# Kernel optimization log

Hardware: AMD Instinct MI355X
Metric: run time of the kernel (lower is better)

Reference implementation:

```python
import jax, jax.numpy as jnp
import numpy as np

MARGIN = 0.3
EPS = 1e-12

def setup_inputs() -> dict:
    key = jax.random.key(0)
    k1, k2 = jax.random.split(key)
    B, D, NUM_IDS = 1024, 2048, 256
    features = jax.random.normal(k1, (B, D), dtype=jnp.float32)
    labels = jax.random.randint(k2, (B,), 0, NUM_IDS, dtype=jnp.int64)
    return {"features": features, "labels": labels}

def _pairwise_euclidean(features):
    # dist^2 = |x_i|^2 + |x_j|^2 - 2 x_i . x_j, clamped then sqrt (as in torch ref)
    sq = jnp.sum(features * features, axis=1)  # [B]
    d2 = sq[:, None] + sq[None, :] - 2.0 * (features @ features.T)
    return jnp.sqrt(jnp.maximum(d2, EPS))

def reference(features, labels):
    B = features.shape[0]
    dist = _pairwise_euclidean(features)  # [B, B]
    eq = labels[None, :] == labels[:, None]  # [B, B]; eq[i] == labels_equal row i
    eye = jnp.eye(B, dtype=bool)
    pos_mask = eq & ~eye
    neg_mask = ~eq
    neg_inf = jnp.float32(-jnp.inf)
    pos_inf = jnp.float32(jnp.inf)
    hardest_pos = jnp.max(jnp.where(pos_mask, dist, neg_inf), axis=1)  # [B]
    hardest_neg = jnp.min(jnp.where(neg_mask, dist, pos_inf), axis=1)  # [B]
    valid = jnp.any(pos_mask, axis=1) & jnp.any(neg_mask, axis=1)  # rows contributing a triplet
    per_row = jax.nn.relu(hardest_pos - hardest_neg + MARGIN)
    per_row = jnp.where(valid, per_row, 0.0)
    n_valid = jnp.sum(valid)
    loss = jnp.sum(per_row) / jnp.maximum(n_valid, 1).astype(per_row.dtype)
    num_active = jnp.sum(valid & (per_row > 0))
    return loss, num_active
```

## Files before the change

### kernel.cpp

```cpp
#include <hip/hip_runtime.h>
#include <math.h>

#define B_SZ 1024
#define D_SZ 2048
#define MARGIN 0.3f

typedef _Float16 f16x8 __attribute__((ext_vector_type(8)));
typedef float f32x16 __attribute__((ext_vector_type(16)));

union FragU { uint4 u; f16x8 v; };
union H4 { _Float16 h[4]; uint2 u; };

#define AS1 __attribute__((address_space(1)))
#define AS3 __attribute__((address_space(3)))



__global__ __launch_bounds__(256) void prep_kernel(const float* __restrict__ F,
                                                   _Float16* __restrict__ Fh,
                                                   float* __restrict__ sqpart,
                                                   int* __restrict__ hp,
                                                   int* __restrict__ hn,
                                                   int* __restrict__ flags) {
    __shared__ _Float16 slab[64][136];
    __shared__ float part[64];

    const int b = blockIdx.x;
    const int i = b >> 4;
    const int kseg = b & 15;
    const int t = threadIdx.x;
    const int lane = t & 63;
    const int w = t >> 6;

    const int idx = b * 256 + t;
    if (idx < 1024) {
        hp[idx] = 0;
        hn[idx] = 0x7F800000;
        flags[idx] = 0;
    }

#pragma unroll
    for (int q = 0; q < 8; ++q) {
        const int rl = q * 8 + (t >> 5);
        const int c4 = (t & 31) * 4;
        const float4 v = *(const float4*)(F + (size_t)(i * 64 + rl) * D_SZ +
                                          kseg * 128 + c4);
        float s = v.x * v.x + v.y * v.y + v.z * v.z + v.w * v.w;
#pragma unroll
        for (int mask = 1; mask < 32; mask <<= 1) s += __shfl_xor(s, mask);
        if ((t & 31) == 0) part[rl] = s;
        H4 p;
        p.h[0] = (_Float16)v.x; p.h[1] = (_Float16)v.y;
        p.h[2] = (_Float16)v.z; p.h[3] = (_Float16)v.w;
        *(uint2*)&slab[rl][c4] = p.u;
    }
    __syncthreads();

    if (t < 64) sqpart[kseg * 1024 + i * 64 + t] = part[t];

#pragma unroll
    for (int q2 = 0; q2 < 4; ++q2) {
        const int u = w * 4 + q2;
        const int kb = u >> 1;
        const int rg = u & 1;
        const uint4 d = *(const uint4*)&slab[rg * 32 + (lane & 31)]
                                          [kb * 16 + (lane >> 5) * 8];
        const size_t g = (size_t)((i * 128 + kseg * 8 + kb) * 2 + rg);
        *(uint4*)((char*)Fh + g * 1024 + (size_t)lane * 16) = d;
    }
}


#define WAVE_STAGE (3 * 8192)

__global__ __launch_bounds__(256) void dist_f16_kernel(
    const _Float16* __restrict__ Fh, const int* __restrict__ labels,
    const float* __restrict__ sqpart, int* __restrict__ hp,
    int* __restrict__ hn, int* __restrict__ flags) {
    __shared__ __align__(16) char stage[4 * WAVE_STAGE];
    __shared__ int labR[64], labC[64];
    __shared__ float sqR[64], sqC[64];

    const int t = threadIdx.x;
    const int lane = t & 63;
    const int w = t >> 6;

    const int tileId = (blockIdx.x & 7) * 32 + (blockIdx.x >> 3);
    const int bi = tileId >> 4;
    const int bj = tileId & 15;
    const int rowBase = bi * 64, colBase = bj * 64;

    if (t < 128) {
        const int e = t & 63;
        const int side = t >> 6;
        const int row = (side ? colBase : rowBase) + e;
        float s = 0.f;
#pragma unroll
        for (int p = 0; p < 16; ++p) s += sqpart[p * 1024 + row];
        if (side) { sqC[e] = s; labC[e] = labels[row]; }
        else      { sqR[e] = s; labR[e] = labels[row]; }
    }
    __syncthreads();
    asm volatile("s_waitcnt vmcnt(0)" ::: "memory");

    const char* __restrict__ FhB = (const char*)Fh;
    char* wbase = stage + w * WAVE_STAGE;
    const char* rbase = wbase + lane * 16;

    f32x16 acc[2][2];
#pragma unroll
    for (int a = 0; a < 2; ++a)
#pragma unroll
        for (int c = 0; c < 2; ++c)
#pragma unroll
            for (int e = 0; e < 16; ++e) acc[a][c][e] = 0.f;

    auto ISSUE = [&](int s, int b) {
        const int kb16 = w * 32 + s * 2;
        const size_t aOff = (size_t)((bi * 128 + kb16) * 2) * 1024 + (size_t)lane * 16;
        const size_t bOff = (size_t)((bj * 128 + kb16) * 2) * 1024 + (size_t)lane * 16;
        char* dA = wbase + b * 8192;
#pragma unroll
        for (int c = 0; c < 4; ++c)
            __builtin_amdgcn_global_load_lds(
                (const AS1 void*)(FhB + aOff + c * 1024),
                (AS3 void*)(dA + c * 1024), 16, 0, 0);
#pragma unroll
        for (int c = 0; c < 4; ++c)
            __builtin_amdgcn_global_load_lds(
                (const AS1 void*)(FhB + bOff + c * 1024),
                (AS3 void*)(dA + 4096 + c * 1024), 16, 0, 0);
    };
    auto COMPUTE = [&](int b) {
        const char* rb = rbase + b * 8192;
#pragma unroll
        for (int kl = 0; kl < 2; ++kl) {
            FragU a0, a1, v0, v1;
            a0.u = *(const uint4*)(rb + (kl * 2 + 0) * 1024);
            a1.u = *(const uint4*)(rb + (kl * 2 + 1) * 1024);
            v0.u = *(const uint4*)(rb + 4096 + (kl * 2 + 0) * 1024);
            v1.u = *(const uint4*)(rb + 4096 + (kl * 2 + 1) * 1024);
            acc[0][0] = __builtin_amdgcn_mfma_f32_32x32x16_f16(a0.v, v0.v, acc[0][0], 0, 0, 0);
            acc[0][1] = __builtin_amdgcn_mfma_f32_32x32x16_f16(a0.v, v1.v, acc[0][1], 0, 0, 0);
            acc[1][0] = __builtin_amdgcn_mfma_f32_32x32x16_f16(a1.v, v0.v, acc[1][0], 0, 0, 0);
            acc[1][1] = __builtin_amdgcn_mfma_f32_32x32x16_f16(a1.v, v1.v, acc[1][1], 0, 0, 0);
        }
    };

#define WAIT16 asm volatile("s_waitcnt vmcnt(16)" ::: "memory"); __builtin_amdgcn_sched_barrier(0)
#define WAIT8  asm volatile("s_waitcnt vmcnt(8)"  ::: "memory"); __builtin_amdgcn_sched_barrier(0)
#define WAIT0  asm volatile("s_waitcnt vmcnt(0)"  ::: "memory"); __builtin_amdgcn_sched_barrier(0)

    ISSUE(0, 0);
    ISSUE(1, 1);
    for (int s3 = 0; s3 < 12; s3 += 3) {
        ISSUE(s3 + 2, 2); WAIT16; COMPUTE(0);
        ISSUE(s3 + 3, 0); WAIT16; COMPUTE(1);
        ISSUE(s3 + 4, 1); WAIT16; COMPUTE(2);
    }
    ISSUE(14, 2); WAIT16; COMPUTE(0);
    ISSUE(15, 0); WAIT16; COMPUTE(1);
    WAIT8;  COMPUTE(2);
    WAIT0;  COMPUTE(0);

#undef WAIT16
#undef WAIT8
#undef WAIT0

    __syncthreads();

    char* cb = stage;
#pragma unroll
    for (int fr = 0; fr < 2; ++fr)
#pragma unroll
        for (int fc = 0; fc < 2; ++fc)
#pragma unroll
            for (int g = 0; g < 4; ++g) {
                float4 v;
                v.x = acc[fr][fc][g * 4 + 0];
                v.y = acc[fr][fc][g * 4 + 1];
                v.z = acc[fr][fc][g * 4 + 2];
                v.w = acc[fr][fc][g * 4 + 3];
                *(float4*)(cb + ((size_t)((w * 16 + (fr * 2 + fc) * 4 + g) * 64 + lane)) * 16) = v;
            }
    __syncthreads();

    const int fr = w >> 1, fc = w & 1;
    float cS[16];
#pragma unroll
    for (int e = 0; e < 16; ++e) cS[e] = 0.f;
#pragma unroll
    for (int wp = 0; wp < 4; ++wp)
#pragma unroll
        for (int g = 0; g < 4; ++g) {
            float4 v = *(const float4*)(cb + ((size_t)((wp * 16 + w * 4 + g) * 64 + lane)) * 16);
            cS[g * 4 + 0] += v.x;
            cS[g * 4 + 1] += v.y;
            cS[g * 4 + 2] += v.z;
            cS[g * 4 + 3] += v.w;
        }

    const float BIG = 1e38f;
    const int h = lane >> 5;
    const int colL = fc * 32 + (lane & 31);
    const int j = colBase + colL;
    const int lj = labC[colL];
    const float sqj = sqC[colL];
#pragma unroll
    for (int k = 0; k < 16; ++k) {
        const int rowL = fr * 32 + (k & 3) + 8 * (k >> 2) + 4 * h;
        const int i = rowBase + rowL;
        const float d2 = sqR[rowL] + sqj - 2.f * cS[k];
        const float d = sqrtf(fmaxf(d2, 1e-12f));
        const bool eq = (labR[rowL] == lj);
        const bool isPos = eq && (i != j);
        float pv = isPos ? d : -BIG;
        float nv = eq ? BIG : d;
        int pf = (isPos ? 1 : 0) | (eq ? 0 : 2);
#pragma unroll
        for (int mask = 1; mask < 32; mask <<= 1) {
            pv = fmaxf(pv, __shfl_xor(pv, mask));
            nv = fminf(nv, __shfl_xor(nv, mask));
            pf |= __shfl_xor(pf, mask);
        }
        if ((lane & 31) == 0) {
            if (pf & 1) atomicMax(&hp[i], __float_as_int(pv));
            if (pf & 2) atomicMin(&hn[i], __float_as_int(nv));
            if (pf) atomicOr(&flags[i], pf);
        }
    }
}


__global__ __launch_bounds__(1024) void final_kernel(const int* __restrict__ hp,
                                                     const int* __restrict__ hn,
                                                     const int* __restrict__ flags,
                                                     float* __restrict__ out) {
    __shared__ float ssum[16];
    __shared__ int svalid[16], sact[16];
    const int t = threadIdx.x;
    const float hpv = __int_as_float(hp[t]);
    const float hnv = __int_as_float(hn[t]);
    const int f = flags[t];
    const bool valid = (f == 3);
    float pr = fmaxf(hpv - hnv + MARGIN, 0.f);
    if (!valid) pr = 0.f;
    int act = (valid && pr > 0.f) ? 1 : 0;
    int vld = valid ? 1 : 0;
    float s = pr;
    for (int off = 32; off; off >>= 1) {
        s += __shfl_down(s, off);
        act += __shfl_down(act, off);
        vld += __shfl_down(vld, off);
    }
    if ((t & 63) == 0) {
        ssum[t >> 6] = s;
        svalid[t >> 6] = vld;
        sact[t >> 6] = act;
    }
    __syncthreads();
    if (t == 0) {
        float tot = 0.f;
        int nv = 0, na = 0;
#pragma unroll
        for (int i = 0; i < 16; ++i) {
            tot += ssum[i];
            nv += svalid[i];
            na += sact[i];
        }
        out[0] = tot / (float)(nv > 1 ? nv : 1);
        out[1] = (float)na;
    }
}


#define BM 64
#define BN 64
#define BK 32

__global__ __launch_bounds__(256) void sq_kernel(const float* __restrict__ F,
                                                 float* __restrict__ sq) {
    int row = blockIdx.x;
    const float4* r4 = (const float4*)(F + (size_t)row * D_SZ);
    int t = threadIdx.x;
    float s = 0.f;
#pragma unroll
    for (int q = 0; q < 2; ++q) {
        float4 v = r4[t + q * 256];
        s += v.x * v.x + v.y * v.y + v.z * v.z + v.w * v.w;
    }
    for (int off = 32; off; off >>= 1) s += __shfl_down(s, off);
    __shared__ float wsum[4];
    if ((t & 63) == 0) wsum[t >> 6] = s;
    __syncthreads();
    if (t == 0) sq[row] = wsum[0] + wsum[1] + wsum[2] + wsum[3];
}

__global__ __launch_bounds__(256) void init_kernel(int* __restrict__ hp,
                                                   int* __restrict__ hn,
                                                   int* __restrict__ flags) {
    int i = blockIdx.x * 256 + threadIdx.x;
    hp[i] = 0;
    hn[i] = 0x7F800000;
    flags[i] = 0;
}

__global__ __launch_bounds__(256) void dist_f32_kernel(
    const float* __restrict__ F, const int* __restrict__ labels,
    const float* __restrict__ sq, int* __restrict__ hp, int* __restrict__ hn,
    int* __restrict__ flags) {
    __shared__ float As[BK][BM];
    __shared__ float Bs[BK][BN];
    __shared__ int labR[BM], labC[BN];
    __shared__ float sqR[BM], sqC[BN];

    const int rowBase = blockIdx.y * BM;
    const int colBase = blockIdx.x * BN;
    const int t = threadIdx.x;
    const int tx = t & 15;
    const int ty = t >> 4;

    if (t < 64) {
        labR[t] = labels[rowBase + t];
        sqR[t] = sq[rowBase + t];
    } else if (t < 128) {
        int u = t - 64;
        labC[u] = labels[colBase + u];
        sqC[u] = sq[colBase + u];
    }

    float acc[4][4] = {{0.f}};
    const int m = t & 63;
    const int q = t >> 6;
    const float* aRow = F + (size_t)(rowBase + m) * D_SZ + q * 8;
    const float* bRow = F + (size_t)(colBase + m) * D_SZ + q * 8;

    for (int k0 = 0; k0 < D_SZ; k0 += BK) {
        float4 a0 = *(const float4*)(aRow + k0);
        float4 a1 = *(const float4*)(aRow + k0 + 4);
        float4 b0 = *(const float4*)(bRow + k0);
        float4 b1 = *(const float4*)(bRow + k0 + 4);
        __syncthreads();
        int kb = q * 8;
        As[kb + 0][m] = a0.x; As[kb + 1][m] = a0.y;
        As[kb + 2][m] = a0.z; As[kb + 3][m] = a0.w;
        As[kb + 4][m] = a1.x; As[kb + 5][m] = a1.y;
        As[kb + 6][m] = a1.z; As[kb + 7][m] = a1.w;
        Bs[kb + 0][m] = b0.x; Bs[kb + 1][m] = b0.y;
        Bs[kb + 2][m] = b0.z; Bs[kb + 3][m] = b0.w;
        Bs[kb + 4][m] = b1.x; Bs[kb + 5][m] = b1.y;
        Bs[kb + 6][m] = b1.z; Bs[kb + 7][m] = b1.w;
        __syncthreads();
#pragma unroll
        for (int kk = 0; kk < BK; ++kk) {
            float4 a = *(const float4*)&As[kk][ty * 4];
            float4 b = *(const float4*)&Bs[kk][tx * 4];
            acc[0][0] += a.x * b.x; acc[0][1] += a.x * b.y;
            acc[0][2] += a.x * b.z; acc[0][3] += a.x * b.w;
            acc[1][0] += a.y * b.x; acc[1][1] += a.y * b.y;
            acc[1][2] += a.y * b.z; acc[1][3] += a.y * b.w;
            acc[2][0] += a.z * b.x; acc[2][1] += a.z * b.y;
            acc[2][2] += a.z * b.z; acc[2][3] += a.z * b.w;
            acc[3][0] += a.w * b.x; acc[3][1] += a.w * b.y;
            acc[3][2] += a.w * b.z; acc[3][3] += a.w * b.w;
        }
    }

    float mp[4], mn[4];
    int pf[4];
#pragma unroll
    for (int rr = 0; rr < 4; ++rr) {
        const int i = rowBase + ty * 4 + rr;
        const int li = labR[ty * 4 + rr];
        const float si = sqR[ty * 4 + rr];
        mp[rr] = -3.4e38f;
        mn[rr] = 3.4e38f;
        pf[rr] = 0;
#pragma unroll
        for (int c = 0; c < 4; ++c) {
            const int j = colBase + tx * 4 + c;
            const float d2 = si + sqC[tx * 4 + c] - 2.f * acc[rr][c];
            const float dist = sqrtf(fmaxf(d2, 1e-12f));
            const bool eq = (li == labC[tx * 4 + c]);
            if (eq && (i != j)) {
                mp[rr] = fmaxf(mp[rr], dist);
                pf[rr] |= 1;
            }
            if (!eq) {
                mn[rr] = fminf(mn[rr], dist);
                pf[rr] |= 2;
            }
        }
    }
#pragma unroll
    for (int mask = 1; mask < 16; mask <<= 1)
#pragma unroll
        for (int rr = 0; rr < 4; ++rr) {
            mp[rr] = fmaxf(mp[rr], __shfl_xor(mp[rr], mask));
            mn[rr] = fminf(mn[rr], __shfl_xor(mn[rr], mask));
            pf[rr] |= __shfl_xor(pf[rr], mask);
        }
    if (tx == 0) {
#pragma unroll
        for (int rr = 0; rr < 4; ++rr) {
            const int i = rowBase + ty * 4 + rr;
            if (pf[rr] & 1) atomicMax(&hp[i], __float_as_int(mp[rr]));
            if (pf[rr] & 2) atomicMin(&hn[i], __float_as_int(mn[rr]));
            if (pf[rr]) atomicOr(&flags[i], pf[rr]);
        }
    }
}


extern "C" void kernel_launch(void* const* d_in, const int* in_sizes, int n_in,
                              void* d_out, int out_size, void* d_ws, size_t ws_size,
                              hipStream_t stream) {
    const float* F = (const float*)d_in[0];
    const int* labels = (const int*)d_in[1];
    float* out = (float*)d_out;
    char* ws = (char*)d_ws;

    const size_t FH = (size_t)B_SZ * D_SZ * 2;
    const size_t SQP = 16 * 1024 * sizeof(float);
    const size_t need = FH + SQP + 12 * 1024;

    if (ws_size >= need) {
        _Float16* Fh = (_Float16*)ws;
        float* sqpart = (float*)(ws + FH);
        char* tail = ws + FH + SQP;
        int* hp = (int*)tail;
        int* hn = (int*)(tail + 4096);
        int* flags = (int*)(tail + 8192);

        prep_kernel<<<256, 256, 0, stream>>>(F, Fh, sqpart, hp, hn, flags);
        dist_f16_kernel<<<256, 256, 0, stream>>>(Fh, labels, sqpart, hp, hn, flags);
        final_kernel<<<1, 1024, 0, stream>>>(hp, hn, flags, out);
    } else {
        float* sq = (float*)ws;
        int* hp = (int*)(ws + 4096);
        int* hn = (int*)(ws + 8192);
        int* flags = (int*)(ws + 12288);

        sq_kernel<<<B_SZ, 256, 0, stream>>>(F, sq);
        init_kernel<<<B_SZ / 256, 256, 0, stream>>>(hp, hn, flags);
        dim3 grid(B_SZ / BN, B_SZ / BM);
        dist_f32_kernel<<<grid, 256, 0, stream>>>(F, labels, sq, hp, hn, flags);
        final_kernel<<<1, 1024, 0, stream>>>(hp, hn, flags, out);
    }
}
```

Baseline: 31.97 us.

## Split distance tiles to 64x32 and launch 512 blocks with XCD-aware mapping

The distance kernel now computes 64x32 output tiles instead of 64x64, doubling the grid to 512 blocks for better occupancy across CUs. The B-operand staging shrinks to half a fragment pair, LDS stage per wave drops, and wait counts are adjusted. The block-to-tile mapping groups tiles per XCD to improve L2 reuse of row panels. The trade-off is that A-panel loads are duplicated across twice as many blocks and MFMA work per loaded byte falls, and only two waves do the epilogue.

Result: no change. 32.41 us (+1.4%).

```diff
diff --git a/kernel.cpp b/kernel.cpp
--- a/kernel.cpp
+++ b/kernel.cpp
@@ -71,34 +71,41 @@
 }
 
 
-#define WAVE_STAGE (3 * 8192)
+#define WAVE_STAGE (3 * 6144)
 
 __global__ __launch_bounds__(256) void dist_f16_kernel(
     const _Float16* __restrict__ Fh, const int* __restrict__ labels,
     const float* __restrict__ sqpart, int* __restrict__ hp,
     int* __restrict__ hn, int* __restrict__ flags) {
     __shared__ __align__(16) char stage[4 * WAVE_STAGE];
-    __shared__ int labR[64], labC[64];
-    __shared__ float sqR[64], sqC[64];
+    __shared__ int labR[64], labC[32];
+    __shared__ float sqR[64], sqC[32];
 
     const int t = threadIdx.x;
     const int lane = t & 63;
     const int w = t >> 6;
 
-    const int tileId = (blockIdx.x & 7) * 32 + (blockIdx.x >> 3);
-    const int bi = tileId >> 4;
-    const int bj = tileId & 15;
-    const int rowBase = bi * 64, colBase = bj * 64;
-
-    if (t < 128) {
-        const int e = t & 63;
-        const int side = t >> 6;
-        const int row = (side ? colBase : rowBase) + e;
+    const int xcd = blockIdx.x & 7;
+    const int cidx = blockIdx.x >> 3;
+    const int bi = (xcd >> 1) * 4 + (cidx >> 4);
+    const int bj = (xcd & 1) * 16 + (cidx & 15);
+    const int rowBase = bi * 64, colBase = bj * 32;
+
+    if (t < 64) {
+        const int row = rowBase + t;
         float s = 0.f;
 #pragma unroll
         for (int p = 0; p < 16; ++p) s += sqpart[p * 1024 + row];
-        if (side) { sqC[e] = s; labC[e] = labels[row]; }
-        else      { sqR[e] = s; labR[e] = labels[row]; }
+        sqR[t] = s;
+        labR[t] = labels[row];
+    } else if (t < 96) {
+        const int e = t - 64;
+        const int row = colBase + e;
+        float s = 0.f;
+#pragma unroll
+        for (int p = 0; p < 16; ++p) s += sqpart[p * 1024 + row];
+        sqC[e] = s;
+        labC[e] = labels[row];
     }
     __syncthreads();
     asm volatile("s_waitcnt vmcnt(0)" ::: "memory");
@@ -107,64 +114,61 @@
     char* wbase = stage + w * WAVE_STAGE;
     const char* rbase = wbase + lane * 16;
 
-    f32x16 acc[2][2];
+    f32x16 acc[2];
 #pragma unroll
     for (int a = 0; a < 2; ++a)
 #pragma unroll
-        for (int c = 0; c < 2; ++c)
-#pragma unroll
-            for (int e = 0; e < 16; ++e) acc[a][c][e] = 0.f;
+        for (int e = 0; e < 16; ++e) acc[a][e] = 0.f;
 
     auto ISSUE = [&](int s, int b) {
         const int kb16 = w * 32 + s * 2;
         const size_t aOff = (size_t)((bi * 128 + kb16) * 2) * 1024 + (size_t)lane * 16;
-        const size_t bOff = (size_t)((bj * 128 + kb16) * 2) * 1024 + (size_t)lane * 16;
-        char* dA = wbase + b * 8192;
+        const size_t bOff = (size_t)(((bj >> 1) * 128 + kb16) * 2 + (bj & 1)) * 1024 +
+                            (size_t)lane * 16;
+        char* dA = wbase + b * 6144;
 #pragma unroll
         for (int c = 0; c < 4; ++c)
             __builtin_amdgcn_global_load_lds(
                 (const AS1 void*)(FhB + aOff + c * 1024),
                 (AS3 void*)(dA + c * 1024), 16, 0, 0);
-#pragma unroll
-        for (int c = 0; c < 4; ++c)
-            __builtin_amdgcn_global_load_lds(
-                (const AS1 void*)(FhB + bOff + c * 1024),
-                (AS3 void*)(dA + 4096 + c * 1024), 16, 0, 0);
+        __builtin_amdgcn_global_load_lds(
+            (const AS1 void*)(FhB + bOff),
+            (AS3 void*)(dA + 4096), 16, 0, 0);
+        __builtin_amdgcn_global_load_lds(
+            (const AS1 void*)(FhB + bOff + 2048),
+            (AS3 void*)(dA + 5120), 16, 0, 0);
     };
     auto COMPUTE = [&](int b) {
-        const char* rb = rbase + b * 8192;
+        const char* rb = rbase + b * 6144;
 #pragma unroll
         for (int kl = 0; kl < 2; ++kl) {
-            FragU a0, a1, v0, v1;
+            FragU a0, a1, v0;
             a0.u = *(const uint4*)(rb + (kl * 2 + 0) * 1024);
             a1.u = *(const uint4*)(rb + (kl * 2 + 1) * 1024);
-            v0.u = *(const uint4*)(rb + 4096 + (kl * 2 + 0) * 1024);
-            v1.u = *(const uint4*)(rb + 4096 + (kl * 2 + 1) * 1024);
-            acc[0][0] = __builtin_amdgcn_mfma_f32_32x32x16_f16(a0.v, v0.v, acc[0][0], 0, 0, 0);
-            acc[0][1] = __builtin_amdgcn_mfma_f32_32x32x16_f16(a0.v, v1.v, acc[0][1], 0, 0, 0);
-            acc[1][0] = __builtin_amdgcn_mfma_f32_32x32x16_f16(a1.v, v0.v, acc[1][0], 0, 0, 0);
-            acc[1][1] = __builtin_amdgcn_mfma_f32_32x32x16_f16(a1.v, v1.v, acc[1][1], 0, 0, 0);
+            v0.u = *(const uint4*)(rb + 4096 + kl * 1024);
+            acc[0] = __builtin_amdgcn_mfma_f32_32x32x16_f16(a0.v, v0.v, acc[0], 0, 0, 0);
+            acc[1] = __builtin_amdgcn_mfma_f32_32x32x16_f16(a1.v, v0.v, acc[1], 0, 0, 0);
         }
     };
 
-#define WAIT16 asm volatile("s_waitcnt vmcnt(16)" ::: "memory"); __builtin_amdgcn_sched_barrier(0)
-#define WAIT8  asm volatile("s_waitcnt vmcnt(8)"  ::: "memory"); __builtin_amdgcn_sched_barrier(0)
+#define WAIT12 asm volatile("s_waitcnt vmcnt(12)" ::: "memory"); __builtin_amdgcn_sched_barrier(0)
+#define WAIT6  asm volatile("s_waitcnt vmcnt(6)"  ::: "memory"); __builtin_amdgcn_sched_barrier(0)
 #define WAIT0  asm volatile("s_waitcnt vmcnt(0)"  ::: "memory"); __builtin_amdgcn_sched_barrier(0)
 
     ISSUE(0, 0);
     ISSUE(1, 1);
     for (int s3 = 0; s3 < 12; s3 += 3) {
-        ISSUE(s3 + 2, 2); WAIT16; COMPUTE(0);
-        ISSUE(s3 + 3, 0); WAIT16; COMPUTE(1);
-        ISSUE(s3 + 4, 1); WAIT16; COMPUTE(2);
-    }
-    ISSUE(14, 2); WAIT16; COMPUTE(0);
-    ISSUE(15, 0); WAIT16; COMPUTE(1);
-    WAIT8;  COMPUTE(2);
+        ISSUE(s3 + 2, 2); WAIT12; COMPUTE(0);
+        ISSUE(s3 + 3, 0); WAIT12; COMPUTE(1);
+        ISSUE(s3 + 4, 1); WAIT12; COMPUTE(2);
+    }
+    ISSUE(14, 2); WAIT12; COMPUTE(0);
+    ISSUE(15, 0); WAIT12; COMPUTE(1);
+    WAIT6;  COMPUTE(2);
     WAIT0;  COMPUTE(0);
 
-#undef WAIT16
-#undef WAIT8
+#undef WAIT12
+#undef WAIT6
 #undef WAIT0
 
     __syncthreads();
@@ -173,60 +177,62 @@
 #pragma unroll
     for (int fr = 0; fr < 2; ++fr)
 #pragma unroll
-        for (int fc = 0; fc < 2; ++fc)
+        for (int g = 0; g < 4; ++g) {
+            float4 v;
+            v.x = acc[fr][g * 4 + 0];
+            v.y = acc[fr][g * 4 + 1];
+            v.z = acc[fr][g * 4 + 2];
+            v.w = acc[fr][g * 4 + 3];
+            *(float4*)(cb + (size_t)(w * 8192) +
+                       (size_t)((fr * 4 + g) * 64 + lane) * 16) = v;
+        }
+    __syncthreads();
+
+    if (w < 2) {
+        const int fr = w;
+        float cS[16];
+#pragma unroll
+        for (int e = 0; e < 16; ++e) cS[e] = 0.f;
+#pragma unroll
+        for (int wp = 0; wp < 4; ++wp)
 #pragma unroll
             for (int g = 0; g < 4; ++g) {
-                float4 v;
-                v.x = acc[fr][fc][g * 4 + 0];
-                v.y = acc[fr][fc][g * 4 + 1];
-                v.z = acc[fr][fc][g * 4 + 2];
-                v.w = acc[fr][fc][g * 4 + 3];
-                *(float4*)(cb + ((size_t)((w * 16 + (fr * 2 + fc) * 4 + g) * 64 + lane)) * 16) = v;
+                float4 v = *(const float4*)(cb + (size_t)(wp * 8192) +
+                                            (size_t)((fr * 4 + g) * 64 + lane) * 16);
+                cS[g * 4 + 0] += v.x;
+                cS[g * 4 + 1] += v.y;
+                cS[g * 4 + 2] += v.z;
+                cS[g * 4 + 3] += v.w;
             }
-    __syncthreads();
-
-    const int fr = w >> 1, fc = w & 1;
-    float cS[16];
-#pragma unroll
-    for (int e = 0; e < 16; ++e) cS[e] = 0.f;
-#pragma unroll
-    for (int wp = 0; wp < 4; ++wp)
-#pragma unroll
-        for (int g = 0; g < 4; ++g) {
-            float4 v = *(const float4*)(cb + ((size_t)((wp * 16 + w * 4 + g) * 64 + lane)) * 16);
-            cS[g * 4 + 0] += v.x;
-            cS[g * 4 + 1] += v.y;
-            cS[g * 4 + 2] += v.z;
-            cS[g * 4 + 3] += v.w;
-        }
-
-    const float BIG = 1e38f;
-    const int h = lane >> 5;
-    const int colL = fc * 32 + (lane & 31);
-    const int j = colBase + colL;
-    const int lj = labC[colL];
-    const float sqj = sqC[colL];
-#pragma unroll
-    for (int k = 0; k < 16; ++k) {
-        const int rowL = fr * 32 + (k & 3) + 8 * (k >> 2) + 4 * h;
-        const int i = rowBase + rowL;
-        const float d2 = sqR[rowL] + sqj - 2.f * cS[k];
-        const float d = sqrtf(fmaxf(d2, 1e-12f));
-        const bool eq = (labR[rowL] == lj);
-        const bool isPos = eq && (i != j);
-        float pv = isPos ? d : -BIG;
-        float nv = eq ? BIG : d;
-        int pf = (isPos ? 1 : 0) | (eq ? 0 : 2);
-#pragma unroll
-        for (int mask = 1; mask < 32; mask <<= 1) {
-            pv = fmaxf(pv, __shfl_xor(pv, mask));
-            nv = fminf(nv, __shfl_xor(nv, mask));
-            pf |= __shfl_xor(pf, mask);
-        }
-        if ((lane & 31) == 0) {
-            if (pf & 1) atomicMax(&hp[i], __float_as_int(pv));
-            if (pf & 2) atomicMin(&hn[i], __float_as_int(nv));
-            if (pf) atomicOr(&flags[i], pf);
+
+        const float BIG = 1e38f;
+        const int h = lane >> 5;
+        const int colL = lane & 31;
+        const int j = colBase + colL;
+        const int lj = labC[colL];
+        const float sqj = sqC[colL];
+#pragma unroll
+        for (int k = 0; k < 16; ++k) {
+            const int rowL = fr * 32 + (k & 3) + 8 * (k >> 2) + 4 * h;
+            const int i = rowBase + rowL;
+            const float d2 = sqR[rowL] + sqj - 2.f * cS[k];
+            const float d = sqrtf(fmaxf(d2, 1e-12f));
+            const bool eq = (labR[rowL] == lj);
+            const bool isPos = eq && (i != j);
+            float pv = isPos ? d : -BIG;
+            float nv = eq ? BIG : d;
+            int pf = (isPos ? 1 : 0) | (eq ? 0 : 2);
+#pragma unroll
+            for (int mask = 1; mask < 32; mask <<= 1) {
+                pv = fmaxf(pv, __shfl_xor(pv, mask));
+                nv = fminf(nv, __shfl_xor(nv, mask));
+                pf |= __shfl_xor(pf, mask);
+            }
+            if (colL == 0) {
+                if (pf & 1) atomicMax(&hp[i], __float_as_int(pv));
+                if (pf & 2) atomicMin(&hn[i], __float_as_int(nv));
+                if (pf) atomicOr(&flags[i], pf);
+            }
         }
     }
 }
@@ -433,7 +439,7 @@
         int* flags = (int*)(tail + 8192);
 
         prep_kernel<<<256, 256, 0, stream>>>(F, Fh, sqpart, hp, hn, flags);
-        dist_f16_kernel<<<256, 256, 0, stream>>>(Fh, labels, sqpart, hp, hn, flags);
+        dist_f16_kernel<<<512, 256, 0, stream>>>(Fh, labels, sqpart, hp, hn, flags);
         final_kernel<<<1, 1024, 0, stream>>>(hp, hn, flags, out);
     } else {
         float* sq = (float*)ws;
```
